# Kernel optimization log

Hardware: AMD Instinct MI355X
Metric: run time of the kernel (lower is better)

The kernel has to match this reference:

```python
import jax, jax.numpy as jnp
import numpy as np

C = 2048
EPS = 1e-12


def conv1x1(x, w, b):
    # x: [B,C_in,H,W], w: [C_out,C_in], b: [C_out]
    return jnp.einsum('oc,bchw->bohw', w, x) + b[None, :, None, None]


def unfold3x3(x):
    # torch F.unfold(kernel=3, padding=1): output [B, C*9, H*W],
    # feature order (c, ki, kj) with c slowest.
    B, Cc, H, W = x.shape
    xp = jnp.pad(x, ((0, 0), (0, 0), (1, 1), (1, 1)))
    patches = jnp.stack([xp[:, :, ki:ki + H, kj:kj + W]
                         for ki in range(3) for kj in range(3)], axis=2)  # [B,C,9,H,W]
    return patches.reshape(B, Cc * 9, H * W)


def fold3x3(u, H, W):
    # torch F.fold(kernel=3, padding=1): overlap-add. u: [B, C*9, H*W]
    B = u.shape[0]
    Cc = u.shape[1] // 9
    t = u.reshape(B, Cc, 3, 3, H, W)
    out = jnp.zeros((B, Cc, H + 2, W + 2), dtype=u.dtype)
    for ki in range(3):
        for kj in range(3):
            out = out.at[:, :, ki:ki + H, kj:kj + W].add(t[:, :, ki, kj])
    return out[:, :, 1:1 + H, 1:1 + W]


def l2norm(x, axis):
    n = jnp.sqrt(jnp.sum(x * x, axis=axis, keepdims=True))
    return x / jnp.maximum(n, EPS)


def setup_inputs() -> dict:
    key = jax.random.key(0)
    ks = jax.random.split(key, 8)
    B, H, W = 4, 24, 24
    s = 0.02
    return {
        'part_ref': jax.random.normal(ks[0], (B, C, H, W), jnp.float32),
        'part_target': jax.random.normal(ks[1], (B, C, H, W), jnp.float32),
        'wq': jax.random.normal(ks[2], (C, C), jnp.float32) * s,
        'bq': jnp.zeros((C,), jnp.float32),
        'wk': jax.random.normal(ks[3], (C, C), jnp.float32) * s,
        'bk': jnp.zeros((C,), jnp.float32),
        'wt': jax.random.normal(ks[4], (C, 2 * C), jnp.float32) * s,
        'bt': jnp.zeros((C,), jnp.float32),
    }


def reference(part_ref, part_target, wq, bq, wk, bk, wt, bt):
    B, _, H, W = part_ref.shape
    part_target_o = part_target
    k = conv1x1(part_ref, wk, bk)
    q = conv1x1(part_target, wq, bq)

    tgt_unf = unfold3x3(q)        # [B, C*9, L]
    ref_unf1 = unfold3x3(k)       # [B, C*9, L]

    ref_n = l2norm(jnp.transpose(ref_unf1, (0, 2, 1)), axis=2)  # [B, L, C*9]
    tgt_n = l2norm(tgt_unf, axis=1)                              # [B, C*9, L]

    R = jnp.einsum('blc,bcm->blm', ref_n, tgt_n)  # [B, L_ref, L_tgt]
    R_star = jnp.max(R, axis=1)                   # [B, L]
    R_arg = jnp.argmax(R, axis=1)                 # [B, L]

    # gather best ref patch per target location along dim 2
    T_unf = jnp.take_along_axis(ref_unf1, R_arg[:, None, :], axis=2)  # [B, C*9, L]
    T_part = fold3x3(T_unf, H, W) / 9.0

    S = R_star.reshape(B, 1, H, W)
    x_res = jnp.concatenate((q, T_part), axis=1)  # [B, 2C, H, W]
    res = conv1x1(x_res, wt, bt) * S + part_target_o
    return res
```

## Files before the change

### kernel.cpp

```cpp
#include <hip/hip_runtime.h>
#include <cstddef>
#include <cstdint>

#define LPIX 576
#define CCH  2048
#define NB   4

typedef __attribute__((ext_vector_type(8))) short short8;
typedef __attribute__((ext_vector_type(16))) float f32x16;
typedef __attribute__((ext_vector_type(4))) unsigned short u16x4;

__device__ __forceinline__ unsigned short f2bf(float f) {
    uint32_t u = __builtin_bit_cast(uint32_t, f);
    u += 0x7fff + ((u >> 16) & 1);
    return (unsigned short)(u >> 16);
}
__device__ __forceinline__ float bf2f(unsigned short s) {
    return __builtin_bit_cast(float, (uint32_t)s << 16);
}

__device__ __forceinline__ void gload_lds16(const void* g, void* l) {
    __builtin_amdgcn_global_load_lds((const __attribute__((address_space(1))) void*)g,
                                     (__attribute__((address_space(3))) void*)l, 16, 0, 0);
}

#define ROW32(r, h) (((r) & 3) + 8 * ((r) >> 2) + 4 * (h))

template<int BM, int BN, int FM, int FN>
__device__ __forceinline__ void mm32_core(
    const short* __restrict__ Ab, int lda,
    const short* __restrict__ Bb, int ldb,
    int k0, int kend, short* As, short* Bs,
    int m0, int n0, f32x16 (&acc)[FM][FN])
{
    constexpr int NA  = BM * 8 / 256;
    constexpr int NBC = BN * 8 / 256;
    const int tid  = threadIdx.x;
    const int lane = tid & 63;
    const int w    = tid >> 6;
    const int wr   = w & 1, wc = w >> 1;
    const int u31  = lane & 31;
    const int h    = lane >> 5;

    const short* Aptr[NA]; short* Alds[NA];
    #pragma unroll
    for (int t = 0; t < NA; ++t) {
        const int c = t * 256 + tid;
        const int row = c >> 3, sl = c & 7;
        Aptr[t] = Ab + (size_t)(m0 + row) * lda + ((sl ^ (row & 7)) * 8);
        Alds[t] = As + c * 8;
    }
    const short* Bptr[NBC]; short* Blds[NBC];
    #pragma unroll
    for (int t = 0; t < NBC; ++t) {
        const int c = t * 256 + tid;
        const int row = c >> 3, sl = c & 7;
        Bptr[t] = Bb + (size_t)(n0 + row) * ldb + ((sl ^ (row & 7)) * 8);
        Blds[t] = Bs + c * 8;
    }

    for (int c0 = k0; c0 < kend; c0 += 64) {
        #pragma unroll
        for (int t = 0; t < NA; ++t)  gload_lds16(Aptr[t] + c0, Alds[t]);
        #pragma unroll
        for (int t = 0; t < NBC; ++t) gload_lds16(Bptr[t] + c0, Blds[t]);
        __syncthreads();
        #pragma unroll
        for (int t4 = 0; t4 < 4; ++t4) {
            const int g = 2 * t4 + h;
            short8 fa[FM], fb[FN];
            #pragma unroll
            for (int i = 0; i < FM; ++i) {
                const int row = wr * 32 * FM + i * 32 + u31;
                fa[i] = *(const short8*)(As + row * 64 + ((g ^ (row & 7)) * 8));
            }
            #pragma unroll
            for (int j = 0; j < FN; ++j) {
                const int row = wc * 32 * FN + j * 32 + u31;
                fb[j] = *(const short8*)(Bs + row * 64 + ((g ^ (row & 7)) * 8));
            }
            #pragma unroll
            for (int i = 0; i < FM; ++i)
                #pragma unroll
                for (int j = 0; j < FN; ++j)
                    acc[i][j] = __builtin_amdgcn_mfma_f32_32x32x16_bf16(fa[i], fb[j], acc[i][j], 0, 0, 0);
        }
        __syncthreads();
    }
}

__global__ __launch_bounds__(256) void wcast2_k(const float* __restrict__ wq,
                                                const float* __restrict__ wk,
                                                short* __restrict__ Wb) {
    const float* W = blockIdx.y ? wk : wq;
    short* D = Wb + (size_t)blockIdx.y * CCH * CCH;
    int i = (blockIdx.x * 256 + threadIdx.x) * 4;
    float4 v = *(const float4*)(W + i);
    u16x4 u;
    u.x = f2bf(v.x); u.y = f2bf(v.y); u.z = f2bf(v.z); u.w = f2bf(v.w);
    *(u16x4*)(D + i) = u;
}

__global__ __launch_bounds__(256) void wcast_k(const float* __restrict__ W,
                                               short* __restrict__ Wb) {
    int i = (blockIdx.x * 256 + threadIdx.x) * 4;
    float4 v = *(const float4*)(W + i);
    u16x4 u;
    u.x = f2bf(v.x); u.y = f2bf(v.y); u.z = f2bf(v.z); u.w = f2bf(v.w);
    *(u16x4*)(Wb + i) = u;
}

__global__ __launch_bounds__(256) void tcast_k(const float* __restrict__ tgt,
                                               const float* __restrict__ ref,
                                               short* __restrict__ T1) {
    __shared__ float tile[32][33];
    const int z = blockIdx.z;
    const int b = z & 3, which = z >> 2;
    const float* X = (which ? ref : tgt) + (size_t)b * CCH * LPIX;
    const int c0 = blockIdx.y * 32;
    const int l0 = blockIdx.x * 32;
    const int tx = threadIdx.x, ty = threadIdx.y;
    #pragma unroll
    for (int j = 0; j < 4; ++j)
        tile[ty + j * 8][tx] = X[(size_t)(c0 + ty + j * 8) * LPIX + l0 + tx];
    __syncthreads();
    short* D = T1 + ((size_t)(which * NB + b) * LPIX) * CCH;
    #pragma unroll
    for (int j = 0; j < 4; ++j)
        D[(size_t)(l0 + ty + j * 8) * CCH + c0 + tx] = (short)f2bf(tile[tx][ty + j * 8]);
}

__global__ __launch_bounds__(256) void conv_k(
    const short* __restrict__ T1, const short* __restrict__ Wb,
    const float* __restrict__ bq, const float* __restrict__ bk,
    short* __restrict__ x2t, short* __restrict__ kt,
    float* __restrict__ nq, float* __restrict__ nk)
{
    __shared__ short As[128 * 64];
    __shared__ short Bs[128 * 64];
    const int id = blockIdx.x;
    const int xcd = id & 7, slot = id >> 3;
    const int sid = xcd * 4 + slot / 18;
    const int which = sid >> 4;
    const int n0 = (sid & 15) * 128;
    const int m0 = (slot % 18) * 128;
    const short* Ab = T1 + (size_t)which * (NB * LPIX) * CCH;
    const short* Bb = Wb + (size_t)which * CCH * CCH;
    const float* bias = which ? bk : bq;
    short* Yb = which ? kt : x2t;
    const int ldy = which ? CCH : 4096;
    float* Narr = which ? nk : nq;

    f32x16 acc[2][2] = {};
    mm32_core<128, 128, 2, 2>(Ab, CCH, Bb, CCH, 0, CCH, As, Bs, m0, n0, acc);

    const int lane = threadIdx.x & 63, w = threadIdx.x >> 6;
    const int wr = w & 1, wc = w >> 1;
    const int u31 = lane & 31, h = lane >> 5;
    #pragma unroll
    for (int i = 0; i < 2; ++i) {
        float pv[16];
        #pragma unroll
        for (int r = 0; r < 16; ++r) pv[r] = 0.f;
        #pragma unroll
        for (int j = 0; j < 2; ++j) {
            const int gn = n0 + wc * 64 + j * 32 + u31;
            const float bi = bias[gn];
            #pragma unroll
            for (int r = 0; r < 16; ++r) {
                const int gm = m0 + wr * 64 + i * 32 + ROW32(r, h);
                float v = acc[i][j][r] + bi;
                pv[r] += v * v;
                Yb[(size_t)gm * ldy + gn] = (short)f2bf(v);
            }
        }
        #pragma unroll
        for (int r = 0; r < 16; ++r) {
            float s = pv[r];
            #pragma unroll
            for (int m = 1; m < 32; m <<= 1) s += __shfl_xor(s, m);
            if (u31 == 0) {
                const int gm = m0 + wr * 64 + i * 32 + ROW32(r, h);
                atomicAdd(&Narr[gm], s);
            }
        }
    }
}

__global__ __launch_bounds__(256) void gram_k(
    const short* __restrict__ kt, const short* __restrict__ x2t,
    float* __restrict__ Mpart)
{
    __shared__ short As[64 * 64];
    __shared__ short Bs[64 * 64];
    const int z = blockIdx.z;
    const int b = z >> 1, kc = z & 1;
    const short* Ab = kt + (size_t)b * LPIX * CCH;
    const short* Bb = x2t + (size_t)b * LPIX * 4096;
    const int m0 = blockIdx.y * 64;
    const int n0 = blockIdx.x * 64;
    f32x16 acc[1][1] = {};
    mm32_core<64, 64, 1, 1>(Ab, CCH, Bb, 4096, kc * 1024, kc * 1024 + 1024, As, Bs, m0, n0, acc);
    float* Mb = Mpart + (size_t)(kc * NB + b) * LPIX * LPIX;
    const int lane = threadIdx.x & 63, w = threadIdx.x >> 6;
    const int wr = w & 1, wc = w >> 1;
    const int u31 = lane & 31, h = lane >> 5;
    const int gn = n0 + wc * 32 + u31;
    #pragma unroll
    for (int r = 0; r < 16; ++r) {
        const int gm = m0 + wr * 32 + ROW32(r, h);
        Mb[(size_t)gm * LPIX + gn] = acc[0][0][r];
    }
}

__global__ __launch_bounds__(256) void fin_k(
    const short* __restrict__ wtb, const short* __restrict__ x2t,
    const float* __restrict__ bt, const float* __restrict__ S,
    const float* __restrict__ PT, float* __restrict__ out)
{
    __shared__ short As[128 * 64];
    __shared__ short Bs[128 * 64];
    const int id = blockIdx.x;
    const int xcd = id & 7, slot = id >> 3;
    const int sid = xcd * 4 + slot / 18;
    const int kc = sid >> 4;
    const int m0 = (sid & 15) * 128;
    const int n0 = (slot % 18) * 128;
    f32x16 acc[2][2] = {};
    mm32_core<128, 128, 2, 2>(wtb, 4096, x2t, 4096, kc * 2048, kc * 2048 + 2048,
                              As, Bs, m0, n0, acc);
    const int lane = threadIdx.x & 63, w = threadIdx.x >> 6;
    const int wr = w & 1, wc = w >> 1;
    const int u31 = lane & 31, h = lane >> 5;
    #pragma unroll
    for (int i = 0; i < 2; ++i)
        #pragma unroll
        for (int j = 0; j < 2; ++j) {
            const int gn = n0 + wc * 64 + j * 32 + u31;
            const int bb = gn / LPIX;
            const int l  = gn - bb * LPIX;
            const float sv = S[gn];
            #pragma unroll
            for (int r = 0; r < 16; ++r) {
                const int gm = m0 + wr * 64 + i * 32 + ROW32(r, h);
                const size_t idx = ((size_t)bb * CCH + gm) * LPIX + l;
                float v = kc ? (acc[i][j][r] + bt[gm]) * sv + PT[idx]
                             : acc[i][j][r] * sv;
                atomicAdd(&out[idx], v);
            }
        }
}

__global__ __launch_bounds__(256) void argmax1_k(
    const float* __restrict__ Mpart, const float* __restrict__ nk,
    float* __restrict__ Pv, int* __restrict__ Pi)
{
    const int b   = blockIdx.z;
    const int lrb = blockIdx.y;
    const int tx = threadIdx.x, ty = threadIdx.y;
    const int tid = ty * 64 + tx;
    __shared__ float invNkS[24];
    if (tid < 24) {
        const int jr = tid;
        float s = 0.f;
        #pragma unroll
        for (int di = -1; di <= 1; ++di) {
            const int ii = lrb + di;
            if ((unsigned)ii > 23u) continue;
            #pragma unroll
            for (int dj = -1; dj <= 1; ++dj) {
                const int jj = jr + dj;
                if ((unsigned)jj > 23u) continue;
                s += nk[b * LPIX + ii * 24 + jj];
            }
        }
        invNkS[jr] = 1.0f / fmaxf(sqrtf(s), 1e-12f);
    }
    __syncthreads();
    const int lt = blockIdx.x * 64 + tx;
    const int it = lt / 24, jt = lt % 24;
    const float* Mb0 = Mpart + (size_t)b * LPIX * LPIX;
    const float* Mb1 = Mpart + (size_t)(NB + b) * LPIX * LPIX;
    float best = -1e30f; int bidx = 0;
    #pragma unroll
    for (int i = 0; i < 6; ++i) {
        const int jr = ty + i * 4;
        const int lr = lrb * 24 + jr;
        const int base = lr * LPIX + lt;
        float g = 0.f;
        #pragma unroll
        for (int di = -1; di <= 1; ++di) {
            if ((unsigned)(lrb + di) > 23u || (unsigned)(it + di) > 23u) continue;
            #pragma unroll
            for (int dj = -1; dj <= 1; ++dj) {
                if ((unsigned)(jr + dj) > 23u || (unsigned)(jt + dj) > 23u) continue;
                const int o = base + (di * 24 + dj) * (LPIX + 1);
                g += Mb0[o] + Mb1[o];
            }
        }
        float v = g * invNkS[jr];
        if (v > best) { best = v; bidx = lr; }
    }
    __shared__ float rv[4][64];
    __shared__ int   ri[4][64];
    rv[ty][tx] = best; ri[ty][tx] = bidx;
    __syncthreads();
    if (ty == 0) {
        #pragma unroll
        for (int y = 1; y < 4; ++y) {
            float v = rv[y][tx]; int id = ri[y][tx];
            if (v > best || (v == best && id < bidx)) { best = v; bidx = id; }
        }
        Pv[((size_t)b * 24 + lrb) * LPIX + lt] = best;
        Pi[((size_t)b * 24 + lrb) * LPIX + lt] = bidx;
    }
}

__global__ __launch_bounds__(256) void argmax2_k(
    const float* __restrict__ Pv, const int* __restrict__ Pi,
    const float* __restrict__ nq,
    float* __restrict__ S, int* __restrict__ Arg)
{
    int idx = blockIdx.x * 256 + threadIdx.x;
    if (idx >= NB * LPIX) return;
    int b = idx / LPIX, lt = idx % LPIX;
    int it = lt / 24, jt = lt % 24;
    float s = 0.f;
    #pragma unroll
    for (int di = -1; di <= 1; ++di) {
        const int ii = it + di;
        if ((unsigned)ii > 23u) continue;
        #pragma unroll
        for (int dj = -1; dj <= 1; ++dj) {
            const int jj = jt + dj;
            if ((unsigned)jj > 23u) continue;
            s += nq[b * LPIX + ii * 24 + jj];
        }
    }
    const float invNq = 1.0f / fmaxf(sqrtf(s), 1e-12f);
    float best = -1e30f; int bidx = 0;
    #pragma unroll
    for (int c = 0; c < 24; ++c) {
        float v = Pv[((size_t)b * 24 + c) * LPIX + lt];
        int  id = Pi[((size_t)b * 24 + c) * LPIX + lt];
        if (v > best || (v == best && id < bidx)) { best = v; bidx = id; }
    }
    S[idx]   = best * invNq;
    Arg[idx] = bidx;
}

__global__ __launch_bounds__(256) void gather_k(
    const short* __restrict__ kt, const int* __restrict__ Arg,
    short* __restrict__ x2t)
{
    const int id = blockIdx.x;
    const int xcd = id & 7, slot = id >> 3;
    const int b  = xcd >> 1;
    const int l0 = ((xcd & 1) * 72 + slot) * 4;
    const int lane = threadIdx.x, ty = threadIdx.y;
    const int tid = ty * 64 + lane;
    __shared__ int tap[4][9];
    if (tid < 36) {
        int px = tid / 9, t9 = tid % 9;
        int l = l0 + px;
        int i = l / 24, j = l % 24;
        int ki = t9 / 3, kj = t9 % 3;
        int ip = i + 1 - ki, jp = j + 1 - kj;
        int off = -1;
        if (ip >= 0 && ip < 24 && jp >= 0 && jp < 24) {
            int a = Arg[b * LPIX + ip * 24 + jp];
            int rr = a / 24 + ki - 1;
            int cc = a % 24 + kj - 1;
            if (rr >= 0 && rr < 24 && cc >= 0 && cc < 24) off = rr * 24 + cc;
        }
        tap[px][t9] = off;
    }
    __syncthreads();
    const int l = l0 + ty;
    const short* Kb = kt + (size_t)b * LPIX * CCH;
    short* dst = x2t + ((size_t)b * LPIX + l) * 4096 + CCH;
    int t[9];
    #pragma unroll
    for (int i = 0; i < 9; ++i) t[i] = tap[ty][i];
    const float inv9 = 1.0f / 9.0f;
    #pragma unroll
    for (int j = 0; j < 8; ++j) {
        int c = (lane + j * 64) * 4;
        float s0 = 0.f, s1 = 0.f, s2 = 0.f, s3 = 0.f;
        #pragma unroll
        for (int t9 = 0; t9 < 9; ++t9) {
            int off = t[t9];
            if (off < 0) continue;
            u16x4 u = *(const u16x4*)(Kb + (size_t)off * CCH + c);
            s0 += bf2f(u.x); s1 += bf2f(u.y); s2 += bf2f(u.z); s3 += bf2f(u.w);
        }
        u16x4 o;
        o.x = f2bf(s0 * inv9); o.y = f2bf(s1 * inv9);
        o.z = f2bf(s2 * inv9); o.w = f2bf(s3 * inv9);
        *(u16x4*)(dst + c) = o;
    }
}

extern "C" void kernel_launch(void* const* d_in, const int* in_sizes, int n_in,
                              void* d_out, int out_size, void* d_ws, size_t ws_size,
                              hipStream_t stream) {
    const float* part_ref = (const float*)d_in[0];
    const float* part_tgt = (const float*)d_in[1];
    const float* wq = (const float*)d_in[2];
    const float* bq = (const float*)d_in[3];
    const float* wk = (const float*)d_in[4];
    const float* bk = (const float*)d_in[5];
    const float* wt = (const float*)d_in[6];
    const float* bt = (const float*)d_in[7];
    float* out = (float*)d_out;

    short* wqb2 = (short*)d_ws;
    short* wtb  = wqb2;
    short* T1   = wqb2 + (size_t)2 * CCH * CCH;
    short* kt   = T1 + (size_t)2 * NB * LPIX * CCH;
    short* x2t  = kt + (size_t)NB * LPIX * CCH;
    float* Mpart = (float*)T1;
    float* nk    = (float*)(x2t + (size_t)NB * LPIX * 4096);
    float* nq    = nk + NB * LPIX;
    float* Sbuf  = nq + NB * LPIX;
    int*   Arg   = (int*)(Sbuf + NB * LPIX);
    float* Pv    = (float*)(Arg + NB * LPIX);
    int*   Pi    = (int*)(Pv + (size_t)24 * NB * LPIX);

    hipMemsetAsync(nk, 0, 2 * NB * LPIX * sizeof(float), stream);
    hipMemsetAsync(out, 0, (size_t)NB * CCH * LPIX * sizeof(float), stream);

    wcast2_k<<<dim3(4096, 2), 256, 0, stream>>>(wq, wk, wqb2);
    tcast_k<<<dim3(18, 64, 8), dim3(32, 8), 0, stream>>>(part_tgt, part_ref, T1);

    conv_k<<<576, 256, 0, stream>>>(T1, wqb2, bq, bk, x2t, kt, nq, nk);

    gram_k<<<dim3(9, 9, 8), 256, 0, stream>>>(kt, x2t, Mpart);

    argmax1_k<<<dim3(9, 24, NB), dim3(64, 4), 0, stream>>>(Mpart, nk, Pv, Pi);
    argmax2_k<<<9, 256, 0, stream>>>(Pv, Pi, nq, Sbuf, Arg);

    gather_k<<<576, dim3(64, 4), 0, stream>>>(kt, Arg, x2t);

    wcast_k<<<8192, 256, 0, stream>>>(wt, wtb);
    fin_k<<<576, 256, 0, stream>>>(wtb, x2t, bt, Sbuf, part_tgt, out);
}
```

Measured before the change: 394.1 us.

## Double-buffer LDS tiles in shared bf16 MFMA GEMM core

The shared GEMM core used by the conv, gram and final kernels now keeps two LDS tile buffers per operand. At each K step it reads all fragments for the current buffer into registers, issues the global-to-LDS loads for the next step into the other buffer, and then runs the MFMAs, so memory latency overlaps with compute. This drops one barrier per iteration but doubles LDS use per block and raises register pressure because fragments for all four sub-steps are held at once, which may lower occupancy.

Result: slower. 427.8 us (+8.5%).

```diff
diff --git a/kernel.cpp b/kernel.cpp
--- a/kernel.cpp
+++ b/kernel.cpp
@@ -35,6 +35,8 @@
 {
     constexpr int NA  = BM * 8 / 256;
     constexpr int NBC = BN * 8 / 256;
+    constexpr int ASZ = BM * 64;
+    constexpr int BSZ = BN * 64;
     const int tid  = threadIdx.x;
     const int lane = tid & 63;
     const int w    = tid >> 6;
@@ -59,32 +61,51 @@
         Blds[t] = Bs + c * 8;
     }
 
-    for (int c0 = k0; c0 < kend; c0 += 64) {
-        #pragma unroll
-        for (int t = 0; t < NA; ++t)  gload_lds16(Aptr[t] + c0, Alds[t]);
-        #pragma unroll
-        for (int t = 0; t < NBC; ++t) gload_lds16(Bptr[t] + c0, Blds[t]);
-        __syncthreads();
+    const int nsteps = (kend - k0) >> 6;
+
+    #pragma unroll
+    for (int t = 0; t < NA; ++t)  gload_lds16(Aptr[t] + k0, Alds[t]);
+    #pragma unroll
+    for (int t = 0; t < NBC; ++t) gload_lds16(Bptr[t] + k0, Blds[t]);
+    __syncthreads();
+
+    for (int it = 0; it < nsteps; ++it) {
+        const short* Ac = As + (it & 1) * ASZ;
+        const short* Bc = Bs + (it & 1) * BSZ;
+
+        short8 fa[4][FM], fb[4][FN];
         #pragma unroll
         for (int t4 = 0; t4 < 4; ++t4) {
             const int g = 2 * t4 + h;
-            short8 fa[FM], fb[FN];
             #pragma unroll
             for (int i = 0; i < FM; ++i) {
                 const int row = wr * 32 * FM + i * 32 + u31;
-                fa[i] = *(const short8*)(As + row * 64 + ((g ^ (row & 7)) * 8));
+                fa[t4][i] = *(const short8*)(Ac + row * 64 + ((g ^ (row & 7)) * 8));
             }
             #pragma unroll
             for (int j = 0; j < FN; ++j) {
                 const int row = wc * 32 * FN + j * 32 + u31;
-                fb[j] = *(const short8*)(Bs + row * 64 + ((g ^ (row & 7)) * 8));
-            }
+                fb[t4][j] = *(const short8*)(Bc + row * 64 + ((g ^ (row & 7)) * 8));
+            }
+        }
+
+        if (it + 1 < nsteps) {
+            const int c1 = k0 + (it + 1) * 64;
+            const int nb = (it & 1) ^ 1;
+            #pragma unroll
+            for (int t = 0; t < NA; ++t)  gload_lds16(Aptr[t] + c1, Alds[t] + nb * ASZ);
+            #pragma unroll
+            for (int t = 0; t < NBC; ++t) gload_lds16(Bptr[t] + c1, Blds[t] + nb * BSZ);
+        }
+
+        #pragma unroll
+        for (int t4 = 0; t4 < 4; ++t4)
             #pragma unroll
             for (int i = 0; i < FM; ++i)
                 #pragma unroll
                 for (int j = 0; j < FN; ++j)
-                    acc[i][j] = __builtin_amdgcn_mfma_f32_32x32x16_bf16(fa[i], fb[j], acc[i][j], 0, 0, 0);
-        }
+                    acc[i][j] = __builtin_amdgcn_mfma_f32_32x32x16_bf16(fa[t4][i], fb[t4][j], acc[i][j], 0, 0, 0);
+
         __syncthreads();
     }
 }
@@ -136,8 +157,8 @@
     short* __restrict__ x2t, short* __restrict__ kt,
     float* __restrict__ nq, float* __restrict__ nk)
 {
-    __shared__ short As[128 * 64];
-    __shared__ short Bs[128 * 64];
+    __shared__ short As[2 * 128 * 64];
+    __shared__ short Bs[2 * 128 * 64];
     const int id = blockIdx.x;
     const int xcd = id & 7, slot = id >> 3;
     const int sid = xcd * 4 + slot / 18;
@@ -191,8 +212,8 @@
     const short* __restrict__ kt, const short* __restrict__ x2t,
     float* __restrict__ Mpart)
 {
-    __shared__ short As[64 * 64];
-    __shared__ short Bs[64 * 64];
+    __shared__ short As[2 * 64 * 64];
+    __shared__ short Bs[2 * 64 * 64];
     const int z = blockIdx.z;
     const int b = z >> 1, kc = z & 1;
     const short* Ab = kt + (size_t)b * LPIX * CCH;
@@ -218,8 +239,8 @@
     const float* __restrict__ bt, const float* __restrict__ S,
     const float* __restrict__ PT, float* __restrict__ out)
 {
-    __shared__ short As[128 * 64];
-    __shared__ short Bs[128 * 64];
+    __shared__ short As[2 * 128 * 64];
+    __shared__ short Bs[2 * 128 * 64];
     const int id = blockIdx.x;
     const int xcd = id & 7, slot = id >> 3;
     const int sid = xcd * 4 + slot / 18;
```
